# Optimization experiments

Measured on AMD Instinct MI355X. Metric: run time of the kernel, lower is better.

The kernel has to match this reference:

```python
import jax, jax.numpy as jnp
import numpy as np

DIST_THRESH = 0.5   # stands in for config.dist_thresh
ALPHA = 0.2         # LeakyReLU negative slope
NEG_INF = -9e15     # mask value used by the original module


def setup_inputs() -> dict:
    key = jax.random.key(0)
    k1, k2, k3 = jax.random.split(key, 3)
    N, dim = 8192, 128
    nodes = jax.random.normal(k1, (N, dim), dtype=jnp.float32)
    dist = jax.random.uniform(k2, (N, N), dtype=jnp.float32)
    # xavier_uniform on (2*dim, 1) with gain 1.414
    limit = 1.414 * np.sqrt(6.0 / (2 * dim + 1))
    a = jax.random.uniform(k3, (2 * dim, 1), dtype=jnp.float32,
                           minval=-limit, maxval=limit)
    return {"nodes": nodes, "dist": dist, "a": a}


def reference(nodes, dist, a):
    # Original math: e_ij = leakyrelu([h_i || h_j] @ a). Since a = [a1; a2],
    # this equals leakyrelu(h_i @ a1 + h_j @ a2) — same values, no N^2*2dim tensor.
    dim = nodes.shape[1]
    a1 = a[:dim, 0]                      # [dim]
    a2 = a[dim:, 0]                      # [dim]
    s1 = nodes @ a1                      # [N] — contribution of row node i
    s2 = nodes @ a2                      # [N] — contribution of col node j
    e = jax.nn.leaky_relu(s1[:, None] + s2[None, :], negative_slope=ALPHA)  # [N, N]
    masked = jnp.where(dist < DIST_THRESH, e, NEG_INF)
    attention = jax.nn.softmax(masked, axis=1)   # [N, N]
    h_prime = attention @ nodes                  # [N, dim]
    return h_prime
```

## Files before the change

### kernel.cpp

```cpp
#include <hip/hip_runtime.h>
#include <stdint.h>

#define NN 8192
#define DIM 128
#define ALPHA 0.2f
#define MTILE 32
#define BTHREADS 512
#define BK 256
#define NCHUNK (NN / BK)
#define WSTRIDE (BK + 8)

typedef float f32x16 __attribute__((ext_vector_type(16)));
typedef short bf16x8 __attribute__((ext_vector_type(8)));

__device__ __forceinline__ float b2f(uint32_t u){
  uint32_t x = u << 16;
  float f;
  __builtin_memcpy(&f, &x, 4);
  return f;
}
__device__ __forceinline__ uint16_t f2b(float f){
  uint32_t x;
  __builtin_memcpy(&x, &f, 4);
  x += 0x7FFFu + ((x >> 16) & 1u);
  return (uint16_t)(x >> 16);
}

__global__ void s_kernel(const float* __restrict__ nodes,
                         const float* __restrict__ a,
                         float* __restrict__ s1, float* __restrict__ s2){
  int row  = blockIdx.x * 4 + (threadIdx.x >> 6);
  int lane = threadIdx.x & 63;
  float2 nv  = *(const float2*)(nodes + row * DIM + lane * 2);
  float2 a1v = *(const float2*)(a + lane * 2);
  float2 a2v = *(const float2*)(a + DIM + lane * 2);
  float p1 = nv.x * a1v.x + nv.y * a1v.y;
  float p2 = nv.x * a2v.x + nv.y * a2v.y;
  #pragma unroll
  for (int off = 32; off; off >>= 1){
    p1 += __shfl_down(p1, off);
    p2 += __shfl_down(p2, off);
  }
  if (lane == 0){ s1[row] = p1; s2[row] = p2; }
}

__global__ void t_kernel(const float* __restrict__ nodes,
                         uint16_t* __restrict__ nodesT){
  __shared__ uint16_t tile[32][33];
  int kb = blockIdx.x * 32, nb = blockIdx.y * 32;
  int tx = threadIdx.x & 31, ty = threadIdx.x >> 5;
  for (int r = ty; r < 32; r += 8)
    tile[r][tx] = f2b(nodes[(size_t)(kb + r) * DIM + nb + tx]);
  __syncthreads();
  for (int r = ty; r < 32; r += 8)
    nodesT[(size_t)(nb + r) * NN + kb + tx] = tile[tx][r];
}

__global__ void __launch_bounds__(BTHREADS)
attn_kernel(const float* __restrict__ dist,
            const uint16_t* __restrict__ nodesT,
            const float* __restrict__ s1,
            const float* __restrict__ s2,
            float* __restrict__ out){
  __shared__ uint16_t Wbuf[2][MTILE][WSTRIDE];
  __shared__ float accT[MTILE][DIM];
  __shared__ float denT[MTILE];

  const int tid  = threadIdx.x;
  const int lane = tid & 63;
  const int wave = tid >> 6;
  const int i0   = blockIdx.x * MTILE;

  const int wrow = tid >> 4;
  const int wr   = tid & 15;
  const float s1v = s1[i0 + wrow];
  const float* distRow = dist + (size_t)(i0 + wrow) * NN + wr * 8;

  const int q    = wave & 3;
  const int h    = wave >> 2;
  const int m    = lane & 31;
  const int half = lane >> 5;
  const uint16_t* bRow = nodesT + (size_t)(q * 32 + m) * NN;

  f32x16 acc;
  #pragma unroll
  for (int i = 0; i < 16; i++) acc[i] = 0.f;
  float den = 0.f;

  float4 pd0, pd1, pd2, pd3, ps0, ps1, ps2, ps3;

  auto load_chunk = [&](int s){
    const float* dpp = distRow + s * BK;
    const float* spp = s2 + s * BK + wr * 8;
    pd0 = *(const float4*)(dpp);
    pd1 = *(const float4*)(dpp + 4);
    pd2 = *(const float4*)(dpp + 128);
    pd3 = *(const float4*)(dpp + 132);
    ps0 = *(const float4*)(spp);
    ps1 = *(const float4*)(spp + 4);
    ps2 = *(const float4*)(spp + 128);
    ps3 = *(const float4*)(spp + 132);
  };

  auto gen_write = [&](int buf){
    float dv[16] = {pd0.x, pd0.y, pd0.z, pd0.w, pd1.x, pd1.y, pd1.z, pd1.w,
                    pd2.x, pd2.y, pd2.z, pd2.w, pd3.x, pd3.y, pd3.z, pd3.w};
    float sv[16] = {ps0.x, ps0.y, ps0.z, ps0.w, ps1.x, ps1.y, ps1.z, ps1.w,
                    ps2.x, ps2.y, ps2.z, ps2.w, ps3.x, ps3.y, ps3.z, ps3.w};
    union { bf16x8 v; uint16_t u[8]; } w0, w1;
    #pragma unroll
    for (int j = 0; j < 8; j++){
      float x = s1v + sv[j];
      float e = fmaxf(x, ALPHA * x);
      float w = (dv[j] < 0.5f) ? __expf(e) : 0.f;
      uint16_t wq = f2b(w);
      w0.u[j] = wq;
      den += b2f((uint32_t)wq);
    }
    #pragma unroll
    for (int j = 0; j < 8; j++){
      float x = s1v + sv[8 + j];
      float e = fmaxf(x, ALPHA * x);
      float w = (dv[8 + j] < 0.5f) ? __expf(e) : 0.f;
      uint16_t wq = f2b(w);
      w1.u[j] = wq;
      den += b2f((uint32_t)wq);
    }
    *(bf16x8*)&Wbuf[buf][wrow][wr * 8]       = w0.v;
    *(bf16x8*)&Wbuf[buf][wrow][wr * 8 + 128] = w1.v;
  };

  load_chunk(0);
  gen_write(0);

  for (int s = 0; s < NCHUNK; s++){
    if (s + 1 < NCHUNK) load_chunk(s + 1);
    __syncthreads();
    const int buf = s & 1;
    const size_t kb = (size_t)s * BK;
    #pragma unroll
    for (int kk = 0; kk < 8; kk++){
      int ko = h * 128 + kk * 16 + half * 8;
      bf16x8 av = *(const bf16x8*)&Wbuf[buf][m][ko];
      bf16x8 bv = *(const bf16x8*)(bRow + kb + ko);
      acc = __builtin_amdgcn_mfma_f32_32x32x16_bf16(av, bv, acc, 0, 0, 0);
    }
    if (s + 1 < NCHUNK) gen_write((s + 1) & 1);
  }

  den += __shfl_down(den, 8, 16);
  den += __shfl_down(den, 4, 16);
  den += __shfl_down(den, 2, 16);
  den += __shfl_down(den, 1, 16);
  if (wr == 0) denT[wrow] = 1.0f / den;

  if (h == 0){
    #pragma unroll
    for (int r = 0; r < 16; r++){
      int row = (r & 3) + 8 * (r >> 2) + 4 * half;
      accT[row][q * 32 + m] = acc[r];
    }
  }
  __syncthreads();
  if (h == 1){
    #pragma unroll
    for (int r = 0; r < 16; r++){
      int row = (r & 3) + 8 * (r >> 2) + 4 * half;
      float v = (accT[row][q * 32 + m] + acc[r]) * denT[row];
      out[(size_t)(i0 + row) * DIM + q * 32 + m] = v;
    }
  }
}

extern "C" void kernel_launch(void* const* d_in, const int* in_sizes, int n_in,
                              void* d_out, int out_size, void* d_ws, size_t ws_size,
                              hipStream_t stream){
  const float* nodes = (const float*)d_in[0];
  const float* dist  = (const float*)d_in[1];
  const float* a     = (const float*)d_in[2];
  float* out = (float*)d_out;

  char* ws = (char*)d_ws;
  float*    s1     = (float*)ws;
  float*    s2     = (float*)(ws + (32 << 10));
  uint16_t* nodesT = (uint16_t*)(ws + (64 << 10));

  s_kernel<<<NN / 4, 256, 0, stream>>>(nodes, a, s1, s2);
  t_kernel<<<dim3(NN / 32, DIM / 32), 256, 0, stream>>>(nodes, nodesT);
  attn_kernel<<<NN / MTILE, BTHREADS, 0, stream>>>(dist, nodesT, s1, s2, out);
}
```

Measured before the change: 391.8 us.

## Precompute bit-packed distance mask in separate pass and hoist B-operand loads

A new bandwidth-oriented kernel streams the full fp32 dist matrix once and packs the threshold test into one bit per entry. The attention kernel then reads only 2 bytes per row segment per chunk instead of 64 bytes of dist. The goal is to take the long-latency dist reads out of the low-occupancy MFMA loop. The B-operand global loads are hoisted ahead of the MFMA sequence, and __syncthreads is replaced by an LDS-only wait plus barrier. The cost is an extra kernel launch and a separate full pass over dist, plus a mask buffer in the workspace.

```diff
diff --git a/kernel.cpp b/kernel.cpp
--- a/kernel.cpp
+++ b/kernel.cpp
@@ -24,6 +24,33 @@
   __builtin_memcpy(&x, &f, 4);
   x += 0x7FFFu + ((x >> 16) & 1u);
   return (uint16_t)(x >> 16);
+}
+
+__device__ __forceinline__ void bar_lds(){
+  asm volatile("s_waitcnt lgkmcnt(0)" ::: "memory");
+  __builtin_amdgcn_s_barrier();
+  asm volatile("" ::: "memory");
+}
+
+__global__ void __launch_bounds__(256)
+mask_kernel(const float* __restrict__ dist, uint8_t* __restrict__ mask){
+  const size_t nb = (size_t)NN * NN / 8;
+  const size_t stride = (size_t)gridDim.x * 256;
+  for (size_t f = (size_t)blockIdx.x * 256 + threadIdx.x; f < nb; f += stride){
+    const float* p = dist + f * 8;
+    float4 a = *(const float4*)(p);
+    float4 b = *(const float4*)(p + 4);
+    uint32_t m = 0;
+    m |= (a.x < 0.5f) ? 1u   : 0u;
+    m |= (a.y < 0.5f) ? 2u   : 0u;
+    m |= (a.z < 0.5f) ? 4u   : 0u;
+    m |= (a.w < 0.5f) ? 8u   : 0u;
+    m |= (b.x < 0.5f) ? 16u  : 0u;
+    m |= (b.y < 0.5f) ? 32u  : 0u;
+    m |= (b.z < 0.5f) ? 64u  : 0u;
+    m |= (b.w < 0.5f) ? 128u : 0u;
+    mask[f] = (uint8_t)m;
+  }
 }
 
 __global__ void s_kernel(const float* __restrict__ nodes,
@@ -56,8 +83,8 @@
     nodesT[(size_t)(nb + r) * NN + kb + tx] = tile[tx][r];
 }
 
-__global__ void __launch_bounds__(BTHREADS)
-attn_kernel(const float* __restrict__ dist,
+__global__ void __launch_bounds__(BTHREADS, 4)
+attn_kernel(const uint8_t* __restrict__ mask,
             const uint16_t* __restrict__ nodesT,
             const float* __restrict__ s1,
             const float* __restrict__ s2,
@@ -74,7 +101,7 @@
   const int wrow = tid >> 4;
   const int wr   = tid & 15;
   const float s1v = s1[i0 + wrow];
-  const float* distRow = dist + (size_t)(i0 + wrow) * NN + wr * 8;
+  const uint8_t* mRow = mask + (size_t)(i0 + wrow) * (NN / 8) + wr;
 
   const int q    = wave & 3;
   const int h    = wave >> 2;
@@ -87,15 +114,13 @@
   for (int i = 0; i < 16; i++) acc[i] = 0.f;
   float den = 0.f;
 
-  float4 pd0, pd1, pd2, pd3, ps0, ps1, ps2, ps3;
+  uint32_t mb0, mb1;
+  float4 ps0, ps1, ps2, ps3;
 
   auto load_chunk = [&](int s){
-    const float* dpp = distRow + s * BK;
+    mb0 = mRow[s * 32];
+    mb1 = mRow[s * 32 + 16];
     const float* spp = s2 + s * BK + wr * 8;
-    pd0 = *(const float4*)(dpp);
-    pd1 = *(const float4*)(dpp + 4);
-    pd2 = *(const float4*)(dpp + 128);
-    pd3 = *(const float4*)(dpp + 132);
     ps0 = *(const float4*)(spp);
     ps1 = *(const float4*)(spp + 4);
     ps2 = *(const float4*)(spp + 128);
@@ -103,8 +128,6 @@
   };
 
   auto gen_write = [&](int buf){
-    float dv[16] = {pd0.x, pd0.y, pd0.z, pd0.w, pd1.x, pd1.y, pd1.z, pd1.w,
-                    pd2.x, pd2.y, pd2.z, pd2.w, pd3.x, pd3.y, pd3.z, pd3.w};
     float sv[16] = {ps0.x, ps0.y, ps0.z, ps0.w, ps1.x, ps1.y, ps1.z, ps1.w,
                     ps2.x, ps2.y, ps2.z, ps2.w, ps3.x, ps3.y, ps3.z, ps3.w};
     union { bf16x8 v; uint16_t u[8]; } w0, w1;
@@ -112,7 +135,7 @@
     for (int j = 0; j < 8; j++){
       float x = s1v + sv[j];
       float e = fmaxf(x, ALPHA * x);
-      float w = (dv[j] < 0.5f) ? __expf(e) : 0.f;
+      float w = ((mb0 >> j) & 1u) ? __expf(e) : 0.f;
       uint16_t wq = f2b(w);
       w0.u[j] = wq;
       den += b2f((uint32_t)wq);
@@ -121,7 +144,7 @@
     for (int j = 0; j < 8; j++){
       float x = s1v + sv[8 + j];
       float e = fmaxf(x, ALPHA * x);
-      float w = (dv[8 + j] < 0.5f) ? __expf(e) : 0.f;
+      float w = ((mb1 >> j) & 1u) ? __expf(e) : 0.f;
       uint16_t wq = f2b(w);
       w1.u[j] = wq;
       den += b2f((uint32_t)wq);
@@ -135,15 +158,18 @@
 
   for (int s = 0; s < NCHUNK; s++){
     if (s + 1 < NCHUNK) load_chunk(s + 1);
-    __syncthreads();
+    bar_lds();
     const int buf = s & 1;
     const size_t kb = (size_t)s * BK;
+    bf16x8 bvv[8];
+    #pragma unroll
+    for (int kk = 0; kk < 8; kk++)
+      bvv[kk] = *(const bf16x8*)(bRow + kb + h * 128 + kk * 16 + half * 8);
     #pragma unroll
     for (int kk = 0; kk < 8; kk++){
       int ko = h * 128 + kk * 16 + half * 8;
       bf16x8 av = *(const bf16x8*)&Wbuf[buf][m][ko];
-      bf16x8 bv = *(const bf16x8*)(bRow + kb + ko);
-      acc = __builtin_amdgcn_mfma_f32_32x32x16_bf16(av, bv, acc, 0, 0, 0);
+      acc = __builtin_amdgcn_mfma_f32_32x32x16_bf16(av, bvv[kk], acc, 0, 0, 0);
     }
     if (s + 1 < NCHUNK) gen_write((s + 1) & 1);
   }
@@ -184,8 +210,10 @@
   float*    s1     = (float*)ws;
   float*    s2     = (float*)(ws + (32 << 10));
   uint16_t* nodesT = (uint16_t*)(ws + (64 << 10));
-
+  uint8_t*  mask   = (uint8_t*)(ws + (64 << 10) + (NN * NN / 4));
+
+  mask_kernel<<<2048, 256, 0, stream>>>(dist, mask);
   s_kernel<<<NN / 4, 256, 0, stream>>>(nodes, a, s1, s2);
   t_kernel<<<dim3(NN / 32, DIM / 32), 256, 0, stream>>>(nodes, nodesT);
-  attn_kernel<<<NN / MTILE, BTHREADS, 0, stream>>>(dist, nodesT, s1, s2, out);
-}
+  attn_kernel<<<NN / MTILE, BTHREADS, 0, stream>>>(mask, nodesT, s1, s2, out);
+}
```

New measurement: 448.4 us. +14.4%, slower.
